# Kernel tuning notes

Measured on AMD Instinct MI355X. Metric: run time of the kernel, lower is better.

Reference implementation:

```python
import jax, jax.numpy as jnp
import numpy as np

D_MODEL = 1024
D_FF = 4096
NUM_HEADS = 16
D_HEAD = D_MODEL // NUM_HEADS
EPS = 1e-5


def setup_inputs() -> dict:
    key = jax.random.key(0)
    ks = jax.random.split(key, 16)
    s = 0.02
    return {
        "X": jax.random.normal(ks[0], (2, 2048, D_MODEL), dtype=jnp.float32),
        "W_qkv": jax.random.normal(ks[1], (D_MODEL, 3 * D_MODEL), dtype=jnp.float32) * s,
        "b_qkv": jax.random.normal(ks[2], (3 * D_MODEL,), dtype=jnp.float32) * s,
        "W_o": jax.random.normal(ks[3], (D_MODEL, D_MODEL), dtype=jnp.float32) * s,
        "b_o": jax.random.normal(ks[4], (D_MODEL,), dtype=jnp.float32) * s,
        "W_1": jax.random.normal(ks[5], (D_MODEL, D_FF), dtype=jnp.float32) * s,
        "b_1": jax.random.normal(ks[6], (D_FF,), dtype=jnp.float32) * s,
        "W_2": jax.random.normal(ks[7], (D_FF, D_MODEL), dtype=jnp.float32) * s,
        "b_2": jax.random.normal(ks[8], (D_MODEL,), dtype=jnp.float32) * s,
        "ln1_g": jnp.ones((D_MODEL,), dtype=jnp.float32),
        "ln1_b": jnp.zeros((D_MODEL,), dtype=jnp.float32),
        "ln2_g": jnp.ones((D_MODEL,), dtype=jnp.float32),
        "ln2_b": jnp.zeros((D_MODEL,), dtype=jnp.float32),
    }


def _layernorm(x, g, b):
    mu = jnp.mean(x, axis=-1, keepdims=True)
    var = jnp.mean(jnp.square(x - mu), axis=-1, keepdims=True)
    return (x - mu) * jax.lax.rsqrt(var + EPS) * g + b


def reference(X, W_qkv, b_qkv, W_o, b_o, W_1, b_1, W_2, b_2, ln1_g, ln1_b, ln2_g, ln2_b):
    B, T, D = X.shape
    qkv = X @ W_qkv + b_qkv                      # [B,T,3D]
    Q, K, V = jnp.split(qkv, 3, axis=-1)
    # [B,H,T,d]
    Q = Q.reshape(B, T, NUM_HEADS, D_HEAD).transpose(0, 2, 1, 3)
    K = K.reshape(B, T, NUM_HEADS, D_HEAD).transpose(0, 2, 1, 3)
    V = V.reshape(B, T, NUM_HEADS, D_HEAD).transpose(0, 2, 1, 3)
    scores = jnp.einsum('bhqd,bhkd->bhqk', Q, K) / np.float32(D_HEAD) ** 0.5
    causal = jnp.tril(jnp.ones((T, T), dtype=bool))
    scores = jnp.where(causal, scores, jnp.float32(-jnp.inf))
    A = jax.nn.softmax(scores, axis=-1)
    O = jnp.einsum('bhqk,bhkd->bhqd', A, V)
    O = O.transpose(0, 2, 1, 3).reshape(B, T, D)
    O = O @ W_o + b_o
    H_1 = _layernorm(X + O, ln1_g, ln1_b)
    H_2 = (jax.nn.gelu(H_1 @ W_1 + b_1, approximate=False)) @ W_2 + b_2
    return _layernorm(H_1 + H_2, ln2_g, ln2_b)
```

## Files before the change

kernel.cpp:

```cpp
#include <hip/hip_runtime.h>
#include <cmath>

typedef unsigned short u16;
typedef __bf16 bf16x8 __attribute__((ext_vector_type(8)));
typedef float f32x4 __attribute__((ext_vector_type(4)));

#define DEVI __device__ __forceinline__

DEVI float b2f(u16 u){ union{unsigned int i; float f;} v; v.i=(unsigned int)u<<16; return v.f; }
DEVI u16 f2b(float f){ union{unsigned int i; float f;} v; v.f=f;
    unsigned int r=(v.i+0x7FFFu+((v.i>>16)&1u))>>16; return (u16)r; }

DEVI void gload_lds16(const u16* g, u16* l){
    __builtin_amdgcn_global_load_lds((__attribute__((address_space(1))) void*)g,
                                     (__attribute__((address_space(3))) void*)l,
                                     16, 0, 0);
}

__global__ __launch_bounds__(256)
void cvt_bf16(const float* __restrict__ in, u16* __restrict__ out)
{
    const int i = (blockIdx.x * 256 + threadIdx.x) * 4;
    float4 v = *(const float4*)&in[i];
    ushort4 o;
    o.x = f2b(v.x); o.y = f2b(v.y); o.z = f2b(v.z); o.w = f2b(v.w);
    *(ushort4*)&out[i] = o;
}

__global__ __launch_bounds__(256)
void cvt_transpose(const float* __restrict__ in, u16* __restrict__ out, int R, int C)
{
    __shared__ __align__(16) u16 tile[64*72];
    const int rb = blockIdx.x*64, cb = blockIdx.y*64;
    const int t = threadIdx.x;
    const int r = t >> 3, c0 = (t & 7) * 8;
    #pragma unroll
    for (int rr = 0; rr < 2; rr++) {
        const int row = r + rr*32;
        float4 a = *(const float4*)&in[(long)(rb + row)*C + cb + c0];
        float4 b = *(const float4*)&in[(long)(rb + row)*C + cb + c0 + 4];
        u16* tp = &tile[row*72 + c0];
        tp[0]=f2b(a.x); tp[1]=f2b(a.y); tp[2]=f2b(a.z); tp[3]=f2b(a.w);
        tp[4]=f2b(b.x); tp[5]=f2b(b.y); tp[6]=f2b(b.z); tp[7]=f2b(b.w);
    }
    __syncthreads();
    #pragma unroll
    for (int rr = 0; rr < 2; rr++) {
        const int cr = r + rr*32;
        u16 tmp[8];
        #pragma unroll
        for (int j = 0; j < 8; j++) tmp[j] = tile[(c0 + j)*72 + cr];
        *(uint4*)&out[(long)(cb + cr)*R + rb + c0] = *(uint4*)tmp;
    }
}

template<int EPI, int BM>
__global__ __launch_bounds__(256)
void gemm_bt(const u16* __restrict__ A, const u16* __restrict__ Bt,
             const float* __restrict__ bias, const u16* __restrict__ Res,
             u16* __restrict__ C, u16* __restrict__ C2, int M, int N, int K)
{
    constexpr int RM = BM / 32;
    constexpr int NA = (BM / 16) * 2 / 4;
    __shared__ __align__(16) u16 As[BM*64];
    __shared__ __align__(16) u16 Bs[128*64];
    const int tid  = threadIdx.x;
    const int wave = tid >> 6, lane = tid & 63;
    const int tm = blockIdx.x * BM, tn = blockIdx.y * 128;

    const int rs = lane >> 2, cs = (lane & 3) * 8;
    const u16* gA[NA]; u16* lA[NA];
    #pragma unroll
    for (int i = 0; i < NA; i++) {
        const int c = wave + i*4;
        const int p = c / (BM/16), rb = c % (BM/16);
        gA[i] = A + (long)(tm + rb*16 + rs)*K + p*32 + cs;
        lA[i] = As + p*(BM*32) + rb*512;
    }
    const u16* gB[4]; u16* lB[4];
    #pragma unroll
    for (int i = 0; i < 4; i++) {
        const int c = wave + i*4;
        const int p = c >> 3, rb = c & 7;
        gB[i] = Bt + (long)(tn + rb*16 + rs)*K + p*32 + cs;
        lB[i] = Bs + p*(128*32) + rb*512;
    }

    const int wm = (wave >> 1) * (BM/2), wn = (wave & 1) * 64;
    const int fr = lane & 15, fq = lane >> 4;

    f32x4 acc[RM][4] = {};
    for (int k0 = 0; k0 < K; k0 += 64) {
        __syncthreads();
        #pragma unroll
        for (int i = 0; i < NA; i++) gload_lds16(gA[i] + k0, lA[i]);
        #pragma unroll
        for (int i = 0; i < 4; i++)  gload_lds16(gB[i] + k0, lB[i]);
        __syncthreads();
        #pragma unroll
        for (int p = 0; p < 2; p++) {
            bf16x8 af[RM], bfr[4];
            #pragma unroll
            for (int i = 0; i < RM; i++)
                af[i]  = *(const bf16x8*)&As[p*(BM*32) + (wm + i*16 + fr)*32 + fq*8];
            #pragma unroll
            for (int j = 0; j < 4; j++)
                bfr[j] = *(const bf16x8*)&Bs[p*(128*32) + (wn + j*16 + fr)*32 + fq*8];
            #pragma unroll
            for (int i = 0; i < RM; i++)
                #pragma unroll
                for (int j = 0; j < 4; j++)
                    acc[i][j] = __builtin_amdgcn_mfma_f32_16x16x32_bf16(af[i], bfr[j], acc[i][j], 0, 0, 0);
        }
    }

    #pragma unroll
    for (int i = 0; i < RM; i++) {
        const int row = tm + wm + i*16 + fq*4;
        #pragma unroll
        for (int j = 0; j < 4; j++) {
            const int col = tn + wn + j*16 + fr;
            const float bv = bias[col];
            if (EPI == 3 && col >= 2048) {
                const int hh = (col - 2048) >> 6, dd = (col - 2048) & 63;
                const int batch = row >> 11, tok = row & 2047;
                u16 pk[4];
                #pragma unroll
                for (int r = 0; r < 4; r++) pk[r] = f2b(acc[i][j][r] + bv);
                *(uint2*)&C2[((long)(batch*16 + hh)*64 + dd)*2048 + tok] = *(uint2*)pk;
            } else {
                const int cw = (EPI == 3) ? 2048 : N;
                #pragma unroll
                for (int r = 0; r < 4; r++) {
                    float v = acc[i][j][r] + bv;
                    const long idx = (long)(row + r)*cw + col;
                    if (EPI == 1) v += b2f(Res[idx]);
                    if (EPI == 2) {
                        const float u = v + 0.044715f*v*v*v;
                        const float t = exp2f(u * 2.302208f);
                        v = v * t * __builtin_amdgcn_rcpf(t + 1.f);
                    }
                    C[idx] = f2b(v);
                }
            }
        }
    }
}

__global__ __launch_bounds__(256)
void attn_kernel(const u16* __restrict__ QK, const u16* __restrict__ VT,
                 u16* __restrict__ O)
{
    constexpr float CS = 0.18033688011112042f;
    __shared__ __align__(16) u16 Ks[2*128*32];
    __shared__ __align__(16) u16 Vs[4*64*32];
    __shared__ __align__(16) u16 Ps[4*16*64];

    const int tid = threadIdx.x, wave = tid >> 6, lane = tid & 63;
    const int qt = 31 - blockIdx.x, h = blockIdx.y, b = blockIdx.z;
    const int fr = lane & 15, fq = lane >> 4;
    const long qkbase = (long)b*2048*2048;
    const long vtbase = (long)(b*16 + h)*64*2048;

    bf16x8 bq[2];
    #pragma unroll
    for (int ks = 0; ks < 2; ks++)
        bq[ks] = *(const bf16x8*)&QK[qkbase + (long)(qt*64 + wave*16 + fr)*2048
                                     + h*64 + ks*32 + fq*8];

    const int q_glob = qt*64 + wave*16 + fr;
    const int q_wmin = qt*64 + wave*16;
    f32x4 o[4] = {};
    float m_i = -1e30f, l_i = 0.f;
    const int nkt = (qt >> 1) + 1;
    const int rs = lane >> 2, cs2 = (lane & 3) * 8;
    const int sw = (fr & 7) * 8;

    for (int kt = 0; kt < nkt; kt++) {
        const int k0 = kt * 128;
        __syncthreads();
        #pragma unroll
        for (int i = 0; i < 4; i++) {
            const int c = wave + i*4;
            const int kp = c >> 3, krb = c & 7;
            gload_lds16(QK + qkbase + (long)(k0 + krb*16 + rs)*2048
                           + 1024 + h*64 + kp*32 + cs2,
                        Ks + kp*4096 + krb*512);
            const int vp = c & 3, vrb = c >> 2;
            gload_lds16(VT + vtbase + (long)(vrb*16 + rs)*2048 + k0 + vp*32 + cs2,
                        Vs + vp*2048 + vrb*512);
        }
        __syncthreads();

        f32x4 st[8];
        #pragma unroll
        for (int mt = 0; mt < 8; mt++) st[mt] = (f32x4){0.f,0.f,0.f,0.f};
        #pragma unroll
        for (int mt = 0; mt < 8; mt++)
            #pragma unroll
            for (int ks = 0; ks < 2; ks++) {
                bf16x8 ak = *(const bf16x8*)&Ks[ks*4096 + (mt*16 + fr)*32 + fq*8];
                st[mt] = __builtin_amdgcn_mfma_f32_16x16x32_bf16(ak, bq[ks], st[mt], 0, 0, 0);
            }

        float mx = -1e30f;
        if (k0 + 127 > q_wmin) {
            #pragma unroll
            for (int mt = 0; mt < 8; mt++)
                #pragma unroll
                for (int r = 0; r < 4; r++) {
                    const int key = k0 + mt*16 + fq*4 + r;
                    float v = st[mt][r];
                    if (key > q_glob) v = -1e30f;
                    st[mt][r] = v;
                    mx = fmaxf(mx, v);
                }
        } else {
            #pragma unroll
            for (int mt = 0; mt < 8; mt++)
                #pragma unroll
                for (int r = 0; r < 4; r++) mx = fmaxf(mx, st[mt][r]);
        }
        mx = fmaxf(mx, __shfl_xor(mx, 16, 64));
        mx = fmaxf(mx, __shfl_xor(mx, 32, 64));
        const float mnew  = fmaxf(m_i, mx);
        const float alpha = exp2f((m_i - mnew) * CS);
        float ps = 0.f;
        #pragma unroll
        for (int mt = 0; mt < 8; mt++)
            #pragma unroll
            for (int r = 0; r < 4; r++) {
                const float p = exp2f((st[mt][r] - mnew) * CS);
                st[mt][r] = p; ps += p;
            }
        ps += __shfl_xor(ps, 16, 64);
        ps += __shfl_xor(ps, 32, 64);
        l_i = l_i * alpha + ps;
        m_i = mnew;

        #pragma unroll
        for (int dt = 0; dt < 4; dt++)
            #pragma unroll
            for (int r = 0; r < 4; r++) o[dt][r] *= alpha;

        u16* pw = &Ps[wave * 1024];
        #pragma unroll
        for (int half = 0; half < 2; half++) {
            #pragma unroll
            for (int mt2 = 0; mt2 < 4; mt2++)
                #pragma unroll
                for (int d = 0; d < 2; d++) {
                    const int mt = half*4 + mt2;
                    const unsigned pk = (unsigned)f2b(st[mt][2*d]) |
                                        ((unsigned)f2b(st[mt][2*d+1]) << 16);
                    *(unsigned*)&pw[fr*64 + ((mt2*16 + fq*4 + 2*d) ^ sw)] = pk;
                }
            __asm__ volatile("" ::: "memory");
            bf16x8 bp[2];
            #pragma unroll
            for (int kk = 0; kk < 2; kk++)
                bp[kk] = *(const bf16x8*)&pw[fr*64 + ((kk*32 + fq*8) ^ sw)];
            #pragma unroll
            for (int dt = 0; dt < 4; dt++) {
                #pragma unroll
                for (int kk = 0; kk < 2; kk++) {
                    bf16x8 av = *(const bf16x8*)&Vs[(half*2 + kk)*2048
                                                    + (dt*16 + fr)*32 + fq*8];
                    o[dt] = __builtin_amdgcn_mfma_f32_16x16x32_bf16(av, bp[kk], o[dt], 0, 0, 0);
                }
            }
            __asm__ volatile("" ::: "memory");
        }
    }

    const float rl = __builtin_amdgcn_rcpf(l_i);
    const long orow = (long)b*2048 + qt*64 + wave*16 + fr;
    #pragma unroll
    for (int dt = 0; dt < 4; dt++) {
        u16 pk[4];
        #pragma unroll
        for (int r = 0; r < 4; r++) pk[r] = f2b(o[dt][r] * rl);
        *(uint2*)&O[orow*1024 + h*64 + dt*16 + fq*4] = *(uint2*)pk;
    }
}

template<int OUTF32>
__global__ __launch_bounds__(256)
void ln_kernel(const u16* __restrict__ X, const float* __restrict__ G,
               const float* __restrict__ B, void* __restrict__ Yv)
{
    __shared__ float red[8];
    const int tid = threadIdx.x;
    const long row = blockIdx.x;
    const u16* x = X + row*1024;
    ushort4 u = *(const ushort4*)&x[tid*4];
    const float v0 = b2f(u.x), v1 = b2f(u.y), v2 = b2f(u.z), v3 = b2f(u.w);
    float s = v0+v1+v2+v3;
    float q = v0*v0+v1*v1+v2*v2+v3*v3;
    #pragma unroll
    for (int off = 32; off >= 1; off >>= 1) {
        s += __shfl_xor(s, off, 64);
        q += __shfl_xor(q, off, 64);
    }
    const int wv = tid >> 6;
    if ((tid & 63) == 0) { red[wv*2] = s; red[wv*2+1] = q; }
    __syncthreads();
    s = red[0]+red[2]+red[4]+red[6];
    q = red[1]+red[3]+red[5]+red[7];
    const float mu = s * (1.f/1024.f);
    const float rstd = rsqrtf(fmaxf(q*(1.f/1024.f) - mu*mu, 0.f) + 1e-5f);
    float4 g4 = *(const float4*)&G[tid*4];
    float4 b4 = *(const float4*)&B[tid*4];
    const float y0 = (v0-mu)*rstd*g4.x + b4.x;
    const float y1 = (v1-mu)*rstd*g4.y + b4.y;
    const float y2 = (v2-mu)*rstd*g4.z + b4.z;
    const float y3 = (v3-mu)*rstd*g4.w + b4.w;
    if (OUTF32) {
        float4 o = make_float4(y0, y1, y2, y3);
        *(float4*)&((float*)Yv)[row*1024 + tid*4] = o;
    } else {
        ushort4 o;
        o.x = f2b(y0); o.y = f2b(y1); o.z = f2b(y2); o.w = f2b(y3);
        *(ushort4*)&((u16*)Yv)[row*1024 + tid*4] = o;
    }
}

extern "C" void kernel_launch(void* const* d_in, const int* in_sizes, int n_in,
                              void* d_out, int out_size, void* d_ws, size_t ws_size,
                              hipStream_t stream)
{
    const float* X    = (const float*)d_in[0];
    const float* Wqkv = (const float*)d_in[1];
    const float* bqkv = (const float*)d_in[2];
    const float* Wo   = (const float*)d_in[3];
    const float* bo   = (const float*)d_in[4];
    const float* W1   = (const float*)d_in[5];
    const float* b1   = (const float*)d_in[6];
    const float* W2   = (const float*)d_in[7];
    const float* b2   = (const float*)d_in[8];
    const float* g1   = (const float*)d_in[9];
    const float* be1  = (const float*)d_in[10];
    const float* g2   = (const float*)d_in[11];
    const float* be2  = (const float*)d_in[12];
    float* out = (float*)d_out;

    char* ws = (char*)d_ws;
    u16* Xbf   = (u16*)(ws + 0);
    u16* WqkvT = (u16*)(ws + 8388608);
    u16* WoT   = (u16*)(ws + 14680064);
    u16* QK    = (u16*)(ws + 16777216);
    u16* VT    = (u16*)(ws + 33554432);
    u16* AO    = (u16*)(ws + 41943040);
    u16* S1    = (u16*)(ws + 16777216);
    u16* H1    = (u16*)(ws + 0);
    u16* Gbuf  = (u16*)(ws + 8388608);
    u16* S2    = (u16*)(ws + 41943040);
    u16* W1T   = (u16*)d_out;
    u16* W2T   = (u16*)d_out + 4194304;

    cvt_bf16<<<4096, 256, 0, stream>>>(X, Xbf);
    cvt_transpose<<<dim3(16, 48), 256, 0, stream>>>(Wqkv, WqkvT, 1024, 3072);
    cvt_transpose<<<dim3(16, 16), 256, 0, stream>>>(Wo,   WoT,   1024, 1024);
    cvt_transpose<<<dim3(16, 64), 256, 0, stream>>>(W1,   W1T,   1024, 4096);
    cvt_transpose<<<dim3(64, 16), 256, 0, stream>>>(W2,   W2T,   4096, 1024);

    gemm_bt<3,128><<<dim3(32, 24), 256, 0, stream>>>(Xbf, WqkvT, bqkv, nullptr, QK, VT, 4096, 3072, 1024);
    attn_kernel<<<dim3(32, 16, 2), 256, 0, stream>>>(QK, VT, AO);
    gemm_bt<1,64><<<dim3(64, 8), 256, 0, stream>>>(AO, WoT, bo, Xbf, S1, nullptr, 4096, 1024, 1024);
    ln_kernel<0><<<4096, 256, 0, stream>>>(S1, g1, be1, H1);
    gemm_bt<2,128><<<dim3(32, 32), 256, 0, stream>>>(H1, W1T, b1, nullptr, Gbuf, nullptr, 4096, 4096, 1024);
    gemm_bt<1,64><<<dim3(64, 8), 256, 0, stream>>>(Gbuf, W2T, b2, H1, S2, nullptr, 4096, 1024, 4096);
    ln_kernel<1><<<4096, 256, 0, stream>>>(S2, g2, be2, out);
}
```

Baseline: 407.5 us.

## Double-buffer K/V tiles in attention and shrink key tile to 64

After: 399.6 us. No clear change (-1.9%).

```diff
diff --git a/kernel.cpp b/kernel.cpp
--- a/kernel.cpp
+++ b/kernel.cpp
@@ -152,9 +152,9 @@
                  u16* __restrict__ O)
 {
     constexpr float CS = 0.18033688011112042f;
-    __shared__ __align__(16) u16 Ks[2*128*32];
-    __shared__ __align__(16) u16 Vs[4*64*32];
-    __shared__ __align__(16) u16 Ps[4*16*64];
+    __shared__ __align__(16) u16 Ks[2][4096];
+    __shared__ __align__(16) u16 Vs[2][4096];
+    __shared__ __align__(16) u16 Ps[4][1024];
 
     const int tid = threadIdx.x, wave = tid >> 6, lane = tid & 63;
     const int qt = 31 - blockIdx.x, h = blockIdx.y, b = blockIdx.z;
@@ -172,41 +172,47 @@
     const int q_wmin = qt*64 + wave*16;
     f32x4 o[4] = {};
     float m_i = -1e30f, l_i = 0.f;
-    const int nkt = (qt >> 1) + 1;
+    const int nkt = qt + 1;
     const int rs = lane >> 2, cs2 = (lane & 3) * 8;
     const int sw = (fr & 7) * 8;
 
+    #define ISSUE(bf, k0)                                                      \
+        _Pragma("unroll")                                                      \
+        for (int i = 0; i < 2; i++) {                                          \
+            const int c = wave + i*4;                                          \
+            const int kp = c >> 2, krb = c & 3;                                \
+            gload_lds16(QK + qkbase + (long)((k0) + krb*16 + rs)*2048          \
+                           + 1024 + h*64 + kp*32 + cs2,                        \
+                        &Ks[bf][kp*2048 + krb*512]);                           \
+            const int vp = c & 1, vrb = c >> 1;                                \
+            gload_lds16(VT + vtbase + (long)(vrb*16 + rs)*2048                 \
+                           + (k0) + vp*32 + cs2,                               \
+                        &Vs[bf][vp*2048 + vrb*512]);                           \
+        }
+
+    ISSUE(0, 0)
+
     for (int kt = 0; kt < nkt; kt++) {
-        const int k0 = kt * 128;
+        const int k0 = kt * 64;
+        const int cur = kt & 1;
         __syncthreads();
-        #pragma unroll
-        for (int i = 0; i < 4; i++) {
-            const int c = wave + i*4;
-            const int kp = c >> 3, krb = c & 7;
-            gload_lds16(QK + qkbase + (long)(k0 + krb*16 + rs)*2048
-                           + 1024 + h*64 + kp*32 + cs2,
-                        Ks + kp*4096 + krb*512);
-            const int vp = c & 3, vrb = c >> 2;
-            gload_lds16(VT + vtbase + (long)(vrb*16 + rs)*2048 + k0 + vp*32 + cs2,
-                        Vs + vp*2048 + vrb*512);
-        }
-        __syncthreads();
-
-        f32x4 st[8];
-        #pragma unroll
-        for (int mt = 0; mt < 8; mt++) st[mt] = (f32x4){0.f,0.f,0.f,0.f};
-        #pragma unroll
-        for (int mt = 0; mt < 8; mt++)
+        if (kt + 1 < nkt) { ISSUE(cur ^ 1, k0 + 64) }
+
+        f32x4 st[4];
+        #pragma unroll
+        for (int mt = 0; mt < 4; mt++) st[mt] = (f32x4){0.f,0.f,0.f,0.f};
+        #pragma unroll
+        for (int mt = 0; mt < 4; mt++)
             #pragma unroll
             for (int ks = 0; ks < 2; ks++) {
-                bf16x8 ak = *(const bf16x8*)&Ks[ks*4096 + (mt*16 + fr)*32 + fq*8];
+                bf16x8 ak = *(const bf16x8*)&Ks[cur][ks*2048 + (mt*16 + fr)*32 + fq*8];
                 st[mt] = __builtin_amdgcn_mfma_f32_16x16x32_bf16(ak, bq[ks], st[mt], 0, 0, 0);
             }
 
         float mx = -1e30f;
-        if (k0 + 127 > q_wmin) {
-            #pragma unroll
-            for (int mt = 0; mt < 8; mt++)
+        if (k0 + 63 > q_wmin) {
+            #pragma unroll
+            for (int mt = 0; mt < 4; mt++)
                 #pragma unroll
                 for (int r = 0; r < 4; r++) {
                     const int key = k0 + mt*16 + fq*4 + r;
@@ -217,7 +223,7 @@
                 }
         } else {
             #pragma unroll
-            for (int mt = 0; mt < 8; mt++)
+            for (int mt = 0; mt < 4; mt++)
                 #pragma unroll
                 for (int r = 0; r < 4; r++) mx = fmaxf(mx, st[mt][r]);
         }
@@ -227,7 +233,7 @@
         const float alpha = exp2f((m_i - mnew) * CS);
         float ps = 0.f;
         #pragma unroll
-        for (int mt = 0; mt < 8; mt++)
+        for (int mt = 0; mt < 4; mt++)
             #pragma unroll
             for (int r = 0; r < 4; r++) {
                 const float p = exp2f((st[mt][r] - mnew) * CS);
@@ -243,35 +249,30 @@
             #pragma unroll
             for (int r = 0; r < 4; r++) o[dt][r] *= alpha;
 
-        u16* pw = &Ps[wave * 1024];
-        #pragma unroll
-        for (int half = 0; half < 2; half++) {
-            #pragma unroll
-            for (int mt2 = 0; mt2 < 4; mt2++)
-                #pragma unroll
-                for (int d = 0; d < 2; d++) {
-                    const int mt = half*4 + mt2;
-                    const unsigned pk = (unsigned)f2b(st[mt][2*d]) |
-                                        ((unsigned)f2b(st[mt][2*d+1]) << 16);
-                    *(unsigned*)&pw[fr*64 + ((mt2*16 + fq*4 + 2*d) ^ sw)] = pk;
-                }
-            __asm__ volatile("" ::: "memory");
-            bf16x8 bp[2];
-            #pragma unroll
-            for (int kk = 0; kk < 2; kk++)
-                bp[kk] = *(const bf16x8*)&pw[fr*64 + ((kk*32 + fq*8) ^ sw)];
-            #pragma unroll
-            for (int dt = 0; dt < 4; dt++) {
-                #pragma unroll
-                for (int kk = 0; kk < 2; kk++) {
-                    bf16x8 av = *(const bf16x8*)&Vs[(half*2 + kk)*2048
-                                                    + (dt*16 + fr)*32 + fq*8];
-                    o[dt] = __builtin_amdgcn_mfma_f32_16x16x32_bf16(av, bp[kk], o[dt], 0, 0, 0);
-                }
-            }
-            __asm__ volatile("" ::: "memory");
-        }
-    }
+        u16* pw = Ps[wave];
+        #pragma unroll
+        for (int mt = 0; mt < 4; mt++)
+            #pragma unroll
+            for (int d = 0; d < 2; d++) {
+                const unsigned pk = (unsigned)f2b(st[mt][2*d]) |
+                                    ((unsigned)f2b(st[mt][2*d+1]) << 16);
+                *(unsigned*)&pw[fr*64 + ((mt*16 + fq*4 + 2*d) ^ sw)] = pk;
+            }
+        __asm__ volatile("" ::: "memory");
+        bf16x8 bp[2];
+        #pragma unroll
+        for (int kk = 0; kk < 2; kk++)
+            bp[kk] = *(const bf16x8*)&pw[fr*64 + ((kk*32 + fq*8) ^ sw)];
+        #pragma unroll
+        for (int dt = 0; dt < 4; dt++)
+            #pragma unroll
+            for (int kk = 0; kk < 2; kk++) {
+                bf16x8 av = *(const bf16x8*)&Vs[cur][kk*2048 + (dt*16 + fr)*32 + fq*8];
+                o[dt] = __builtin_amdgcn_mfma_f32_16x16x32_bf16(av, bp[kk], o[dt], 0, 0, 0);
+            }
+        __asm__ volatile("" ::: "memory");
+    }
+    #undef ISSUE
 
     const float rl = __builtin_amdgcn_rcpf(l_i);
     const long orow = (long)b*2048 + qt*64 + wave*16 + fr;
```
